# Kernel tuning notes

Measured on AMD Instinct MI355X. Metric: run time of the kernel, lower is better.

Reference implementation:

```python
import jax, jax.numpy as jnp
import numpy as np

D, DEPTH, H, DH, DF = 768, 12, 12, 64, 3072
INNER = H * DH

def _ln(x, w, b, eps=1e-5):
    mu = jnp.mean(x, axis=-1, keepdims=True)
    var = jnp.var(x, axis=-1, keepdims=True)
    return (x - mu) * jax.lax.rsqrt(var + eps) * w + b

def setup_inputs() -> dict:
    key = jax.random.key(0)
    ks = jax.random.split(key, 12)
    s = lambda k, shape, fan: jax.random.normal(k, shape, jnp.float32) * (fan ** -0.5)
    return {
        "x": jax.random.normal(ks[0], (8, 1024, D), jnp.float32),
        "ln1_w": jnp.ones((DEPTH, D)), "ln1_b": jnp.zeros((DEPTH, D)),
        "w_qkv": s(ks[1], (DEPTH, D, 3 * INNER), D),
        "w_o": s(ks[2], (DEPTH, INNER, D), INNER), "b_o": jnp.zeros((DEPTH, D)),
        "ln2_w": jnp.ones((DEPTH, D)), "ln2_b": jnp.zeros((DEPTH, D)),
        "w1": s(ks[3], (DEPTH, D, DF), D), "b1": jnp.zeros((DEPTH, DF)),
        "w2": s(ks[4], (DEPTH, DF, D), DF), "b2": jnp.zeros((DEPTH, D)),
        "lnf_w": jnp.ones((D,)), "lnf_b": jnp.zeros((D,)),
    }

def reference(x, ln1_w, ln1_b, w_qkv, w_o, b_o, ln2_w, ln2_b, w1, b1, w2, b2, lnf_w, lnf_b):
    scale = DH ** -0.5

    def block(x, p):
        (l1w, l1b, wqkv, wo, bo, l2w, l2b, W1, B1, W2, B2) = p
        h = _ln(x, l1w, l1b)
        qkv = h @ wqkv                              # [b, n, 3*inner]
        q, k, v = jnp.split(qkv, 3, axis=-1)
        rs = lambda t: t.reshape(t.shape[0], t.shape[1], H, DH).transpose(0, 2, 1, 3)
        q, k, v = rs(q), rs(k), rs(v)               # [b, h, n, d]
        dots = jnp.einsum('bhqd,bhkd->bhqk', q, k) * scale
        attn = jax.nn.softmax(dots, axis=-1)
        out = jnp.einsum('bhqk,bhkd->bhqd', attn, v)
        out = out.transpose(0, 2, 1, 3).reshape(x.shape[0], x.shape[1], INNER)
        x = out @ wo + bo + x                       # attn residual
        h = _ln(x, l2w, l2b)
        h = jax.nn.gelu(h @ W1 + B1, approximate=False) @ W2 + B2
        return x + h, None

    params = (ln1_w, ln1_b, w_qkv, w_o, b_o, ln2_w, ln2_b, w1, b1, w2, b2)
    x, _ = jax.lax.scan(block, x, params)
    return _ln(x, lnf_w, lnf_b)
```

## Files before the change

### kernel.cpp

```cpp
#include <hip/hip_runtime.h>
#include <hip/hip_bf16.h>
#include <math.h>

#define BATCH 8
#define SEQ   1024
#define DMODEL 768
#define DEPTH 12
#define NHEAD 12
#define DHEAD 64
#define DFF   3072
#define MROWS (BATCH*SEQ)
#define QKVN  (3*DMODEL)

typedef __attribute__((ext_vector_type(8))) short bf16x8;
typedef __attribute__((ext_vector_type(4))) float f32x4;

__device__ __forceinline__ void gld16(const void* g, void* l) {
    __builtin_amdgcn_global_load_lds(
        (const __attribute__((address_space(1))) void*)g,
        (__attribute__((address_space(3))) void*)l, 16, 0, 0);
}
__device__ __forceinline__ unsigned short bf16b(float f) {
    __hip_bfloat16 hb = __float2bfloat16(f);
    return *(unsigned short*)&hb;
}

template<int BF16OUT>
__global__ __launch_bounds__(256) void ln_kernel(
    const float* __restrict__ in, void* __restrict__ outp,
    const float* __restrict__ w, const float* __restrict__ b)
{
    int row = blockIdx.x;
    const float* x = in + (size_t)row * DMODEL;
    int tid = threadIdx.x;

    float v[3];
    float lsum = 0.f, lsq = 0.f;
#pragma unroll
    for (int i = 0; i < 3; ++i) {
        v[i] = x[tid + i * 256];
        lsum += v[i];
        lsq  += v[i] * v[i];
    }
#pragma unroll
    for (int off = 32; off > 0; off >>= 1) {
        lsum += __shfl_down(lsum, off);
        lsq  += __shfl_down(lsq,  off);
    }
    __shared__ float red[10];
    int wave = tid >> 6, lane = tid & 63;
    if (lane == 0) { red[wave] = lsum; red[wave + 4] = lsq; }
    __syncthreads();
    if (tid == 0) {
        float s = red[0] + red[1] + red[2] + red[3];
        float q = red[4] + red[5] + red[6] + red[7];
        float mu = s * (1.0f / DMODEL);
        float var = q * (1.0f / DMODEL) - mu * mu;
        red[8] = mu;
        red[9] = rsqrtf(var + 1e-5f);
    }
    __syncthreads();
    float mu = red[8], rs = red[9];
#pragma unroll
    for (int i = 0; i < 3; ++i) {
        int c = tid + i * 256;
        float o = (v[i] - mu) * rs * w[c] + b[c];
        if (BF16OUT) ((__hip_bfloat16*)outp)[(size_t)row * DMODEL + c] = __float2bfloat16(o);
        else         ((float*)outp)[(size_t)row * DMODEL + c] = o;
    }
}

__global__ __launch_bounds__(256) void transpose_w(
    const float* __restrict__ W, __hip_bfloat16* __restrict__ Wt, int K, int N)
{
    __shared__ float T[64][65];
    int tid = threadIdx.x;
    int tx = tid & 63, ty = tid >> 6;
    int n0 = blockIdx.x * 64, k0 = blockIdx.y * 64;
#pragma unroll
    for (int i = 0; i < 16; ++i)
        T[ty + 4 * i][tx] = W[(size_t)(k0 + ty + 4 * i) * N + n0 + tx];
    __syncthreads();
#pragma unroll
    for (int i = 0; i < 16; ++i)
        Wt[(size_t)(n0 + ty + 4 * i) * K + k0 + tx] = __float2bfloat16(T[tx][ty + 4 * i]);
}

__global__ __launch_bounds__(256) void transpose_v(
    const __hip_bfloat16* __restrict__ qkv, __hip_bfloat16* __restrict__ vt)
{
    __shared__ unsigned int T[64 * 33];
    int tid = threadIdx.x;
    int s0 = blockIdx.x * 64, h = blockIdx.y, b = blockIdx.z;
    const __hip_bfloat16* src = qkv + ((size_t)(b * SEQ + s0)) * QKVN + 2 * DMODEL + h * DHEAD;
#pragma unroll
    for (int p = 0; p < 2; ++p) {
        int row = (tid >> 3) + 32 * p;
        int c8 = tid & 7;
        uint4 v = *(const uint4*)(src + (size_t)row * QKVN + c8 * 8);
        unsigned int* dst = &T[row * 33 + c8 * 4];
        dst[0] = v.x; dst[1] = v.y; dst[2] = v.z; dst[3] = v.w;
    }
    __syncthreads();
    __hip_bfloat16* ob = vt + ((size_t)(b * NHEAD + h)) * DHEAD * SEQ;
    const unsigned short* Ts = (const unsigned short*)T;
#pragma unroll
    for (int p = 0; p < 2; ++p) {
        int d = (tid >> 3) + 32 * p;
        int sb = (tid & 7) * 8;
        unsigned int wds[4];
#pragma unroll
        for (int j = 0; j < 4; ++j) {
            unsigned int lo = Ts[(size_t)(sb + 2 * j) * 66 + d];
            unsigned int hi = Ts[(size_t)(sb + 2 * j + 1) * 66 + d];
            wds[j] = lo | (hi << 16);
        }
        *(uint4*)(ob + (size_t)d * SEQ + s0 + sb) = *(const uint4*)wds;
    }
}

template<int HAS_BIAS, int ACT_GELU, int HAS_RES, int OUT_BF16>
__global__ __launch_bounds__(256) void gemm_bf16(
    const __hip_bfloat16* __restrict__ A, const __hip_bfloat16* __restrict__ Bt,
    const float* __restrict__ bias, const float* __restrict__ resid,
    void* __restrict__ Cout, int M, int N, int K)
{
    __shared__ __hip_bfloat16 Afr[16 * 512];
    __shared__ __hip_bfloat16 Bfr[16 * 512];

    int tid = threadIdx.x;
    int lane = tid & 63;
    int w = tid >> 6;
    int wm = w >> 1, wn = w & 1;
    int m0 = blockIdx.y * 128;
    int n0 = blockIdx.x * 128;
    int l15 = lane & 15;
    int quad = lane >> 4;

    f32x4 acc[4][4];
#pragma unroll
    for (int i = 0; i < 4; ++i)
#pragma unroll
        for (int j = 0; j < 4; ++j) {
            f32x4 z = {0.f, 0.f, 0.f, 0.f};
            acc[i][j] = z;
        }

    for (int k0 = 0; k0 < K; k0 += 64) {
#pragma unroll
        for (int i = 0; i < 4; ++i) {
            int c = w * 4 + i;
            int row = ((c >> 3) << 6) + ((c & 3) << 4) + l15;
            int kc  = k0 + (((c >> 2) & 1) << 5) + (quad << 3);
            gld16(A  + (size_t)(m0 + row) * K + kc, &Afr[c * 512]);
            gld16(Bt + (size_t)(n0 + row) * K + kc, &Bfr[c * 512]);
        }
        __syncthreads();
#pragma unroll
        for (int t = 0; t < 2; ++t) {
            bf16x8 a[4], b[4];
#pragma unroll
            for (int f = 0; f < 4; ++f) {
                a[f] = *(const bf16x8*)&Afr[(wm * 8 + t * 4 + f) * 512 + lane * 8];
                b[f] = *(const bf16x8*)&Bfr[(wn * 8 + t * 4 + f) * 512 + lane * 8];
            }
#pragma unroll
            for (int i = 0; i < 4; ++i)
#pragma unroll
                for (int j = 0; j < 4; ++j)
                    acc[i][j] = __builtin_amdgcn_mfma_f32_16x16x32_bf16(
                        a[i], b[j], acc[i][j], 0, 0, 0);
        }
        __syncthreads();
    }

#pragma unroll
    for (int i = 0; i < 4; ++i) {
#pragma unroll
        for (int j = 0; j < 4; ++j) {
            int col = n0 + wn * 64 + j * 16 + l15;
            float bv = HAS_BIAS ? bias[col] : 0.f;
#pragma unroll
            for (int r = 0; r < 4; ++r) {
                int row = m0 + wm * 64 + i * 16 + quad * 4 + r;
                float val = acc[i][j][r] + bv;
                if (ACT_GELU) val = 0.5f * val * (1.0f + erff(val * 0.70710678118f));
                if (HAS_RES)  val += resid[(size_t)row * N + col];
                if (OUT_BF16) ((__hip_bfloat16*)Cout)[(size_t)row * N + col] = __float2bfloat16(val);
                else          ((float*)Cout)[(size_t)row * N + col] = val;
            }
        }
    }
}

__global__ __launch_bounds__(256) void fattn_mfma(
    const __hip_bfloat16* __restrict__ qkv,
    const __hip_bfloat16* __restrict__ vt,
    __hip_bfloat16* __restrict__ out)
{
    __shared__ __align__(16) char lds[8192 + 8192 + 4 * 4608];
    char* Kfr = lds;
    char* Vfr = lds + 8192;
    char* Pbase = lds + 16384;

    int tid = threadIdx.x;
    int lane = tid & 63;
    int w = tid >> 6;
    int l15 = lane & 15, quad = lane >> 4;
    int qt = blockIdx.x, h = blockIdx.y, b = blockIdx.z;

    unsigned short* Pw = (unsigned short*)(Pbase + w * 4608);

    const int q0 = qt * 128 + w * 32;
    const __hip_bfloat16* Qp = qkv + ((size_t)(b * SEQ + q0)) * QKVN + h * DHEAD;
    const __hip_bfloat16* Kp = qkv + ((size_t)(b * SEQ)) * QKVN + DMODEL + h * DHEAD;
    const __hip_bfloat16* Vp = vt + ((size_t)(b * NHEAD + h)) * DHEAD * SEQ;

#pragma unroll
    for (int i = 0; i < 4; ++i) {
        int qs = i >> 1, kh = i & 1;
        gld16(Qp + (size_t)(qs * 16 + l15) * QKVN + kh * 32 + quad * 8,
              Pbase + (w * 4 + i) * 1024);
    }
    __syncthreads();
    bf16x8 qf[2][2];
#pragma unroll
    for (int i = 0; i < 4; ++i)
        qf[i >> 1][i & 1] = *(const bf16x8*)(Pbase + (w * 4 + i) * 1024 + lane * 16);

    float m_st[2] = {-1e30f, -1e30f};
    float l_st[2] = {0.f, 0.f};
    f32x4 accO[2][4];
#pragma unroll
    for (int qs = 0; qs < 2; ++qs)
#pragma unroll
        for (int ds = 0; ds < 4; ++ds) {
            f32x4 z = {0.f, 0.f, 0.f, 0.f};
            accO[qs][ds] = z;
        }

    for (int kt = 0; kt < 16; ++kt) {
        __syncthreads();
#pragma unroll
        for (int i = 0; i < 4; ++i) {
            int c = w * 4 + i;
            if (c < 8) {
                gld16(Kp + (size_t)(kt * 64 + ((c >> 1) << 4) + l15) * QKVN
                         + ((c & 1) << 5) + quad * 8,
                      Kfr + c * 1024);
            } else {
                int c2 = c - 8;
                gld16(Vp + (size_t)(((c2 >> 1) << 4) + l15) * SEQ
                         + kt * 64 + ((c2 & 1) << 5) + quad * 8,
                      Vfr + c2 * 1024);
            }
        }
        __syncthreads();

        f32x4 sA[2][4];
#pragma unroll
        for (int qs = 0; qs < 2; ++qs)
#pragma unroll
            for (int ks = 0; ks < 4; ++ks) {
                f32x4 z = {0.f, 0.f, 0.f, 0.f};
                sA[qs][ks] = z;
            }
#pragma unroll
        for (int ks = 0; ks < 4; ++ks)
#pragma unroll
            for (int kh = 0; kh < 2; ++kh) {
                bf16x8 kf = *(const bf16x8*)(Kfr + (ks * 2 + kh) * 1024 + lane * 16);
                sA[0][ks] = __builtin_amdgcn_mfma_f32_16x16x32_bf16(kf, qf[0][kh], sA[0][ks], 0, 0, 0);
                sA[1][ks] = __builtin_amdgcn_mfma_f32_16x16x32_bf16(kf, qf[1][kh], sA[1][ks], 0, 0, 0);
            }

#pragma unroll
        for (int qs = 0; qs < 2; ++qs) {
            float rm = sA[qs][0][0];
#pragma unroll
            for (int ks = 0; ks < 4; ++ks)
#pragma unroll
                for (int r = 0; r < 4; ++r) rm = fmaxf(rm, sA[qs][ks][r]);
            rm = fmaxf(rm, __shfl_xor(rm, 16));
            rm = fmaxf(rm, __shfl_xor(rm, 32));
            float mnew = fmaxf(m_st[qs], rm * 0.125f);
            float alpha = __expf(m_st[qs] - mnew);
            m_st[qs] = mnew;
            float sum = 0.f;
            unsigned short pb[4][4];
#pragma unroll
            for (int ks = 0; ks < 4; ++ks)
#pragma unroll
                for (int r = 0; r < 4; ++r) {
                    float p = __expf(sA[qs][ks][r] * 0.125f - mnew);
                    sum += p;
                    pb[ks][r] = bf16b(p);
                }
            sum += __shfl_xor(sum, 16);
            sum += __shfl_xor(sum, 32);
            l_st[qs] = l_st[qs] * alpha + sum;
#pragma unroll
            for (int ds = 0; ds < 4; ++ds) accO[qs][ds] *= alpha;
#pragma unroll
            for (int ks = 0; ks < 4; ++ks) {
                unsigned int lo = pb[ks][0] | ((unsigned int)pb[ks][1] << 16);
                unsigned int hi = pb[ks][2] | ((unsigned int)pb[ks][3] << 16);
                unsigned int* dst = (unsigned int*)(Pw + (qs * 16 + l15) * 72 + ks * 16 + quad * 4);
                dst[0] = lo; dst[1] = hi;
            }
        }

#pragma unroll
        for (int kh = 0; kh < 2; ++kh) {
            bf16x8 vf[4];
#pragma unroll
            for (int ds = 0; ds < 4; ++ds)
                vf[ds] = *(const bf16x8*)(Vfr + (ds * 2 + kh) * 1024 + lane * 16);
#pragma unroll
            for (int qs = 0; qs < 2; ++qs) {
                bf16x8 pf = *(const bf16x8*)(Pw + (qs * 16 + l15) * 72 + kh * 32 + quad * 8);
#pragma unroll
                for (int ds = 0; ds < 4; ++ds)
                    accO[qs][ds] = __builtin_amdgcn_mfma_f32_16x16x32_bf16(
                        vf[ds], pf, accO[qs][ds], 0, 0, 0);
            }
        }
    }

#pragma unroll
    for (int qs = 0; qs < 2; ++qs) {
        float inv = 1.0f / l_st[qs];
#pragma unroll
        for (int ds = 0; ds < 4; ++ds) {
            unsigned short u[4];
#pragma unroll
            for (int r = 0; r < 4; ++r) u[r] = bf16b(accO[qs][ds][r] * inv);
            unsigned int lo = u[0] | ((unsigned int)u[1] << 16);
            unsigned int hi = u[2] | ((unsigned int)u[3] << 16);
            unsigned int* dst = (unsigned int*)(Pw + (qs * 16 + l15) * 72 + ds * 16 + quad * 4);
            dst[0] = lo; dst[1] = hi;
        }
    }
    __hip_bfloat16* ob = out + ((size_t)(b * SEQ + q0)) * DMODEL + h * DHEAD;
#pragma unroll
    for (int i = 0; i < 4; ++i) {
        int row = i * 8 + (lane >> 3);
        uint4 v = *(const uint4*)(Pw + row * 72 + (lane & 7) * 8);
        *(uint4*)(ob + (size_t)row * DMODEL + (lane & 7) * 8) = v;
    }
}

extern "C" void kernel_launch(void* const* d_in, const int* in_sizes, int n_in,
                              void* d_out, int out_size, void* d_ws, size_t ws_size,
                              hipStream_t stream)
{
    const float* x      = (const float*)d_in[0];
    const float* ln1_w  = (const float*)d_in[1];
    const float* ln1_b  = (const float*)d_in[2];
    const float* w_qkv  = (const float*)d_in[3];
    const float* w_o    = (const float*)d_in[4];
    const float* b_o    = (const float*)d_in[5];
    const float* ln2_w  = (const float*)d_in[6];
    const float* ln2_b  = (const float*)d_in[7];
    const float* w1     = (const float*)d_in[8];
    const float* b1     = (const float*)d_in[9];
    const float* w2     = (const float*)d_in[10];
    const float* b2     = (const float*)d_in[11];
    const float* lnf_w  = (const float*)d_in[12];
    const float* lnf_b  = (const float*)d_in[13];

    char* p = (char*)d_ws;
    float* xbuf = (float*)p;                   p += (size_t)MROWS * DMODEL * 4;
    __hip_bfloat16* qkv  = (__hip_bfloat16*)p; p += (size_t)MROWS * QKVN * 2;
    __hip_bfloat16* hbuf = (__hip_bfloat16*)p; p += (size_t)MROWS * DMODEL * 2;
    __hip_bfloat16* ffn1 = (__hip_bfloat16*)p; p += (size_t)MROWS * DFF * 2;
    __hip_bfloat16* wq_t = (__hip_bfloat16*)p; p += (size_t)QKVN * DMODEL * 2;
    __hip_bfloat16* wo_t = (__hip_bfloat16*)p; p += (size_t)DMODEL * DMODEL * 2;
    __hip_bfloat16* w1_t = (__hip_bfloat16*)p; p += (size_t)DFF * DMODEL * 2;
    __hip_bfloat16* w2_t = (__hip_bfloat16*)p; p += (size_t)DMODEL * DFF * 2;
    __hip_bfloat16* vtb  = (__hip_bfloat16*)p; p += (size_t)MROWS * DMODEL * 2;

    hipMemcpyAsync(xbuf, x, (size_t)MROWS * DMODEL * sizeof(float),
                   hipMemcpyDeviceToDevice, stream);

    for (int l = 0; l < DEPTH; ++l) {
        const float* l1w = ln1_w + (size_t)l * DMODEL;
        const float* l1b = ln1_b + (size_t)l * DMODEL;
        const float* wq  = w_qkv + (size_t)l * DMODEL * QKVN;
        const float* wo  = w_o   + (size_t)l * DMODEL * DMODEL;
        const float* bo  = b_o   + (size_t)l * DMODEL;
        const float* l2w = ln2_w + (size_t)l * DMODEL;
        const float* l2b = ln2_b + (size_t)l * DMODEL;
        const float* W1  = w1    + (size_t)l * DMODEL * DFF;
        const float* B1  = b1    + (size_t)l * DFF;
        const float* W2  = w2    + (size_t)l * DFF * DMODEL;
        const float* B2  = b2    + (size_t)l * DMODEL;

        transpose_w<<<dim3(QKVN / 64, DMODEL / 64), 256, 0, stream>>>(wq, wq_t, DMODEL, QKVN);
        transpose_w<<<dim3(DMODEL / 64, DMODEL / 64), 256, 0, stream>>>(wo, wo_t, DMODEL, DMODEL);
        transpose_w<<<dim3(DFF / 64, DMODEL / 64), 256, 0, stream>>>(W1, w1_t, DMODEL, DFF);
        transpose_w<<<dim3(DMODEL / 64, DFF / 64), 256, 0, stream>>>(W2, w2_t, DFF, DMODEL);

        ln_kernel<1><<<MROWS, 256, 0, stream>>>(xbuf, hbuf, l1w, l1b);
        gemm_bf16<0,0,0,1><<<dim3(QKVN / 128, MROWS / 128), 256, 0, stream>>>(
            hbuf, wq_t, nullptr, nullptr, qkv, MROWS, QKVN, DMODEL);
        transpose_v<<<dim3(SEQ / 64, NHEAD, BATCH), 256, 0, stream>>>(qkv, vtb);
        fattn_mfma<<<dim3(SEQ / 128, NHEAD, BATCH), 256, 0, stream>>>(qkv, vtb, hbuf);
        gemm_bf16<1,0,1,0><<<dim3(DMODEL / 128, MROWS / 128), 256, 0, stream>>>(
            hbuf, wo_t, bo, xbuf, xbuf, MROWS, DMODEL, DMODEL);
        ln_kernel<1><<<MROWS, 256, 0, stream>>>(xbuf, hbuf, l2w, l2b);
        gemm_bf16<1,1,0,1><<<dim3(DFF / 128, MROWS / 128), 256, 0, stream>>>(
            hbuf, w1_t, B1, nullptr, ffn1, MROWS, DFF, DMODEL);
        gemm_bf16<1,0,1,0><<<dim3(DMODEL / 128, MROWS / 128), 256, 0, stream>>>(
            ffn1, w2_t, B2, xbuf, xbuf, MROWS, DMODEL, DFF);
    }

    ln_kernel<0><<<MROWS, 256, 0, stream>>>(xbuf, (float*)d_out, lnf_w, lnf_b);
}
```

Baseline: 4.716 ms.

## Double-buffer LDS tiles in GEMM and flash-attention to overlap loads with MFMA

Both the bf16 GEMM and the flash-attention kernel now keep two LDS buffers and issue the async global-to-LDS loads for the next K tile before running the MFMAs on the current one. This is meant to hide global memory latency and cut one barrier per iteration. The GEMM also precomputes its per-thread load offsets outside the loop. The cost is twice the LDS footprint (GEMM 32KB, attention about 50KB), which can lower occupancy. Correctness depends on the global_load_lds completion being covered by the single barrier at the end of each iteration.

```diff
diff --git a/kernel.cpp b/kernel.cpp
--- a/kernel.cpp
+++ b/kernel.cpp
@@ -125,8 +125,8 @@
     const float* __restrict__ bias, const float* __restrict__ resid,
     void* __restrict__ Cout, int M, int N, int K)
 {
-    __shared__ __hip_bfloat16 Afr[16 * 512];
-    __shared__ __hip_bfloat16 Bfr[16 * 512];
+    __shared__ __hip_bfloat16 Afr[2][16 * 512];
+    __shared__ __hip_bfloat16 Bfr[2][16 * 512];
 
     int tid = threadIdx.x;
     int lane = tid & 63;
@@ -137,6 +137,25 @@
     int l15 = lane & 15;
     int quad = lane >> 4;
 
+    int c0 = w * 4;
+    size_t aoff[4], boff[4];
+#pragma unroll
+    for (int i = 0; i < 4; ++i) {
+        int c = c0 + i;
+        int row = ((c >> 3) << 6) + ((c & 3) << 4) + l15;
+        int kc  = (((c >> 2) & 1) << 5) + (quad << 3);
+        aoff[i] = (size_t)(m0 + row) * K + kc;
+        boff[i] = (size_t)(n0 + row) * K + kc;
+    }
+
+    auto stage = [&](int buf, int k0) {
+#pragma unroll
+        for (int i = 0; i < 4; ++i) {
+            gld16(A  + aoff[i] + k0, &Afr[buf][(c0 + i) * 512]);
+            gld16(Bt + boff[i] + k0, &Bfr[buf][(c0 + i) * 512]);
+        }
+    };
+
     f32x4 acc[4][4];
 #pragma unroll
     for (int i = 0; i < 4; ++i)
@@ -146,23 +165,14 @@
             acc[i][j] = z;
         }
 
-    for (int k0 = 0; k0 < K; k0 += 64) {
-#pragma unroll
-        for (int i = 0; i < 4; ++i) {
-            int c = w * 4 + i;
-            int row = ((c >> 3) << 6) + ((c & 3) << 4) + l15;
-            int kc  = k0 + (((c >> 2) & 1) << 5) + (quad << 3);
-            gld16(A  + (size_t)(m0 + row) * K + kc, &Afr[c * 512]);
-            gld16(Bt + (size_t)(n0 + row) * K + kc, &Bfr[c * 512]);
-        }
-        __syncthreads();
+    auto kstep = [&](int buf) {
 #pragma unroll
         for (int t = 0; t < 2; ++t) {
             bf16x8 a[4], b[4];
 #pragma unroll
             for (int f = 0; f < 4; ++f) {
-                a[f] = *(const bf16x8*)&Afr[(wm * 8 + t * 4 + f) * 512 + lane * 8];
-                b[f] = *(const bf16x8*)&Bfr[(wn * 8 + t * 4 + f) * 512 + lane * 8];
+                a[f] = *(const bf16x8*)&Afr[buf][(wm * 8 + t * 4 + f) * 512 + lane * 8];
+                b[f] = *(const bf16x8*)&Bfr[buf][(wn * 8 + t * 4 + f) * 512 + lane * 8];
             }
 #pragma unroll
             for (int i = 0; i < 4; ++i)
@@ -171,8 +181,19 @@
                     acc[i][j] = __builtin_amdgcn_mfma_f32_16x16x32_bf16(
                         a[i], b[j], acc[i][j], 0, 0, 0);
         }
+    };
+
+    int nsteps = K >> 6;
+    stage(0, 0);
+    __syncthreads();
+    int cur = 0;
+    for (int ks = 1; ks < nsteps; ++ks) {
+        stage(cur ^ 1, ks << 6);
+        kstep(cur);
         __syncthreads();
-    }
+        cur ^= 1;
+    }
+    kstep(cur);
 
 #pragma unroll
     for (int i = 0; i < 4; ++i) {
@@ -198,10 +219,7 @@
     const __hip_bfloat16* __restrict__ vt,
     __hip_bfloat16* __restrict__ out)
 {
-    __shared__ __align__(16) char lds[8192 + 8192 + 4 * 4608];
-    char* Kfr = lds;
-    char* Vfr = lds + 8192;
-    char* Pbase = lds + 16384;
+    __shared__ __align__(16) char lds[2 * 8192 + 2 * 8192 + 4 * 4608];
 
     int tid = threadIdx.x;
     int lane = tid & 63;
@@ -209,6 +227,7 @@
     int l15 = lane & 15, quad = lane >> 4;
     int qt = blockIdx.x, h = blockIdx.y, b = blockIdx.z;
 
+    char* Pbase = lds + 32768;
     unsigned short* Pw = (unsigned short*)(Pbase + w * 4608);
 
     const int q0 = qt * 128 + w * 32;
@@ -216,46 +235,54 @@
     const __hip_bfloat16* Kp = qkv + ((size_t)(b * SEQ)) * QKVN + DMODEL + h * DHEAD;
     const __hip_bfloat16* Vp = vt + ((size_t)(b * NHEAD + h)) * DHEAD * SEQ;
 
-#pragma unroll
-    for (int i = 0; i < 4; ++i) {
-        int qs = i >> 1, kh = i & 1;
-        gld16(Qp + (size_t)(qs * 16 + l15) * QKVN + kh * 32 + quad * 8,
-              Pbase + (w * 4 + i) * 1024);
-    }
-    __syncthreads();
-    bf16x8 qf[2][2];
-#pragma unroll
-    for (int i = 0; i < 4; ++i)
-        qf[i >> 1][i & 1] = *(const bf16x8*)(Pbase + (w * 4 + i) * 1024 + lane * 16);
-
-    float m_st[2] = {-1e30f, -1e30f};
-    float l_st[2] = {0.f, 0.f};
-    f32x4 accO[2][4];
-#pragma unroll
-    for (int qs = 0; qs < 2; ++qs)
-#pragma unroll
-        for (int ds = 0; ds < 4; ++ds) {
-            f32x4 z = {0.f, 0.f, 0.f, 0.f};
-            accO[qs][ds] = z;
-        }
-
-    for (int kt = 0; kt < 16; ++kt) {
-        __syncthreads();
+    auto fstage = [&](int buf, int kt) {
 #pragma unroll
         for (int i = 0; i < 4; ++i) {
             int c = w * 4 + i;
             if (c < 8) {
                 gld16(Kp + (size_t)(kt * 64 + ((c >> 1) << 4) + l15) * QKVN
                          + ((c & 1) << 5) + quad * 8,
-                      Kfr + c * 1024);
+                      lds + buf * 8192 + c * 1024);
             } else {
                 int c2 = c - 8;
                 gld16(Vp + (size_t)(((c2 >> 1) << 4) + l15) * SEQ
                          + kt * 64 + ((c2 & 1) << 5) + quad * 8,
-                      Vfr + c2 * 1024);
-            }
-        }
-        __syncthreads();
+                      lds + 16384 + buf * 8192 + c2 * 1024);
+            }
+        }
+    };
+
+#pragma unroll
+    for (int i = 0; i < 4; ++i) {
+        int qs = i >> 1, kh = i & 1;
+        gld16(Qp + (size_t)(qs * 16 + l15) * QKVN + kh * 32 + quad * 8,
+              Pbase + (w * 4 + i) * 1024);
+    }
+    fstage(0, 0);
+    __syncthreads();
+    bf16x8 qf[2][2];
+#pragma unroll
+    for (int i = 0; i < 4; ++i)
+        qf[i >> 1][i & 1] = *(const bf16x8*)(Pbase + (w * 4 + i) * 1024 + lane * 16);
+    __syncthreads();
+
+    float m_st[2] = {-1e30f, -1e30f};
+    float l_st[2] = {0.f, 0.f};
+    f32x4 accO[2][4];
+#pragma unroll
+    for (int qs = 0; qs < 2; ++qs)
+#pragma unroll
+        for (int ds = 0; ds < 4; ++ds) {
+            f32x4 z = {0.f, 0.f, 0.f, 0.f};
+            accO[qs][ds] = z;
+        }
+
+    int fb = 0;
+    for (int kt = 0; kt < 16; ++kt) {
+        if (kt < 15) fstage(fb ^ 1, kt + 1);
+
+        char* Kfb = lds + fb * 8192;
+        char* Vfb = lds + 16384 + fb * 8192;
 
         f32x4 sA[2][4];
 #pragma unroll
@@ -269,7 +296,7 @@
         for (int ks = 0; ks < 4; ++ks)
 #pragma unroll
             for (int kh = 0; kh < 2; ++kh) {
-                bf16x8 kf = *(const bf16x8*)(Kfr + (ks * 2 + kh) * 1024 + lane * 16);
+                bf16x8 kf = *(const bf16x8*)(Kfb + (ks * 2 + kh) * 1024 + lane * 16);
                 sA[0][ks] = __builtin_amdgcn_mfma_f32_16x16x32_bf16(kf, qf[0][kh], sA[0][ks], 0, 0, 0);
                 sA[1][ks] = __builtin_amdgcn_mfma_f32_16x16x32_bf16(kf, qf[1][kh], sA[1][ks], 0, 0, 0);
             }
@@ -315,7 +342,7 @@
             bf16x8 vf[4];
 #pragma unroll
             for (int ds = 0; ds < 4; ++ds)
-                vf[ds] = *(const bf16x8*)(Vfr + (ds * 2 + kh) * 1024 + lane * 16);
+                vf[ds] = *(const bf16x8*)(Vfb + (ds * 2 + kh) * 1024 + lane * 16);
 #pragma unroll
             for (int qs = 0; qs < 2; ++qs) {
                 bf16x8 pf = *(const bf16x8*)(Pw + (qs * 16 + l15) * 72 + kh * 32 + quad * 8);
@@ -325,6 +352,9 @@
                         vf[ds], pf, accO[qs][ds], 0, 0, 0);
             }
         }
+
+        __syncthreads();
+        fb ^= 1;
     }
 
 #pragma unroll
@@ -380,8 +410,9 @@
     __hip_bfloat16* w2_t = (__hip_bfloat16*)p; p += (size_t)DMODEL * DFF * 2;
     __hip_bfloat16* vtb  = (__hip_bfloat16*)p; p += (size_t)MROWS * DMODEL * 2;
 
-    hipMemcpyAsync(xbuf, x, (size_t)MROWS * DMODEL * sizeof(float),
-                   hipMemcpyDeviceToDevice, stream);
+    hipError_t e = hipMemcpyAsync(xbuf, x, (size_t)MROWS * DMODEL * sizeof(float),
+                                  hipMemcpyDeviceToDevice, stream);
+    (void)e;
 
     for (int l = 0; l < DEPTH; ++l) {
         const float* l1w = ln1_w + (size_t)l * DMODEL;
```

Measured after the change: 5.712 ms. 21.1% more time.

## Double-buffer GEMM LDS tiles with async global-to-LDS prefetch

Applied to the files above, without the earlier changes.

The bf16 GEMM now splits its LDS staging into two 32-wide K buffers and prefetches the next K slice with global_load_lds while running MFMAs on the current one. A partial vmcnt wait and raw s_barrier replace the two __syncthreads per 64-wide step. The goal is to hide global load latency behind matrix math. In exchange there are twice as many loop iterations with half the work each, and correctness depends on the hand-written waitcnt matching the number of outstanding loads.

```diff
diff --git a/kernel.cpp b/kernel.cpp
--- a/kernel.cpp
+++ b/kernel.cpp
@@ -125,8 +125,8 @@
     const float* __restrict__ bias, const float* __restrict__ resid,
     void* __restrict__ Cout, int M, int N, int K)
 {
-    __shared__ __hip_bfloat16 Afr[16 * 512];
-    __shared__ __hip_bfloat16 Bfr[16 * 512];
+    __shared__ __hip_bfloat16 Afr[2][8 * 512];
+    __shared__ __hip_bfloat16 Bfr[2][8 * 512];
 
     int tid = threadIdx.x;
     int lane = tid & 63;
@@ -137,6 +137,24 @@
     int l15 = lane & 15;
     int quad = lane >> 4;
 
+    int ca = w * 2;
+    size_t aoff[2], boff[2];
+#pragma unroll
+    for (int i = 0; i < 2; ++i) {
+        int c = ca + i;
+        int row = ((c >> 2) << 6) + ((c & 3) << 4) + l15;
+        aoff[i] = (size_t)(m0 + row) * K + quad * 8;
+        boff[i] = (size_t)(n0 + row) * K + quad * 8;
+    }
+
+    auto stage = [&](int buf, int k0) {
+#pragma unroll
+        for (int i = 0; i < 2; ++i) {
+            gld16(A  + aoff[i] + k0, &Afr[buf][(ca + i) * 512]);
+            gld16(Bt + boff[i] + k0, &Bfr[buf][(ca + i) * 512]);
+        }
+    };
+
     f32x4 acc[4][4];
 #pragma unroll
     for (int i = 0; i < 4; ++i)
@@ -146,33 +164,37 @@
             acc[i][j] = z;
         }
 
-    for (int k0 = 0; k0 < K; k0 += 64) {
-#pragma unroll
-        for (int i = 0; i < 4; ++i) {
-            int c = w * 4 + i;
-            int row = ((c >> 3) << 6) + ((c & 3) << 4) + l15;
-            int kc  = k0 + (((c >> 2) & 1) << 5) + (quad << 3);
-            gld16(A  + (size_t)(m0 + row) * K + kc, &Afr[c * 512]);
-            gld16(Bt + (size_t)(n0 + row) * K + kc, &Bfr[c * 512]);
-        }
-        __syncthreads();
-#pragma unroll
-        for (int t = 0; t < 2; ++t) {
-            bf16x8 a[4], b[4];
-#pragma unroll
-            for (int f = 0; f < 4; ++f) {
-                a[f] = *(const bf16x8*)&Afr[(wm * 8 + t * 4 + f) * 512 + lane * 8];
-                b[f] = *(const bf16x8*)&Bfr[(wn * 8 + t * 4 + f) * 512 + lane * 8];
-            }
-#pragma unroll
-            for (int i = 0; i < 4; ++i)
-#pragma unroll
-                for (int j = 0; j < 4; ++j)
-                    acc[i][j] = __builtin_amdgcn_mfma_f32_16x16x32_bf16(
-                        a[i], b[j], acc[i][j], 0, 0, 0);
-        }
-        __syncthreads();
-    }
+    auto kstep = [&](int buf) {
+        bf16x8 a[4], b[4];
+#pragma unroll
+        for (int f = 0; f < 4; ++f) {
+            a[f] = *(const bf16x8*)&Afr[buf][(wm * 4 + f) * 512 + lane * 8];
+            b[f] = *(const bf16x8*)&Bfr[buf][(wn * 4 + f) * 512 + lane * 8];
+        }
+#pragma unroll
+        for (int i = 0; i < 4; ++i)
+#pragma unroll
+            for (int j = 0; j < 4; ++j)
+                acc[i][j] = __builtin_amdgcn_mfma_f32_16x16x32_bf16(
+                    a[i], b[j], acc[i][j], 0, 0, 0);
+    };
+
+    int nsteps = K >> 5;
+    stage(0, 0);
+    int cur = 0;
+    for (int ks = 0; ks < nsteps - 1; ++ks) {
+        stage(cur ^ 1, (ks + 1) << 5);
+        asm volatile("s_waitcnt vmcnt(4)" ::: "memory");
+        __builtin_amdgcn_s_barrier();
+        __builtin_amdgcn_sched_barrier(0);
+        kstep(cur);
+        __builtin_amdgcn_s_barrier();
+        cur ^= 1;
+    }
+    asm volatile("s_waitcnt vmcnt(0)" ::: "memory");
+    __builtin_amdgcn_s_barrier();
+    __builtin_amdgcn_sched_barrier(0);
+    kstep(cur);
 
 #pragma unroll
     for (int i = 0; i < 4; ++i) {
@@ -380,8 +402,9 @@
     __hip_bfloat16* w2_t = (__hip_bfloat16*)p; p += (size_t)DMODEL * DFF * 2;
     __hip_bfloat16* vtb  = (__hip_bfloat16*)p; p += (size_t)MROWS * DMODEL * 2;
 
-    hipMemcpyAsync(xbuf, x, (size_t)MROWS * DMODEL * sizeof(float),
-                   hipMemcpyDeviceToDevice, stream);
+    hipError_t e = hipMemcpyAsync(xbuf, x, (size_t)MROWS * DMODEL * sizeof(float),
+                                  hipMemcpyDeviceToDevice, stream);
+    (void)e;
 
     for (int l = 0; l < DEPTH; ++l) {
         const float* l1w = ln1_w + (size_t)l * DMODEL;
```

After: 4.744 ms. Within noise of the previous version (+0.6%).
